# Optimization experiments

Hardware: AMD Instinct MI355X
Metric: run time of the kernel (lower is better)

The kernel has to match this reference:

```python
import jax, jax.numpy as jnp
import numpy as np

IMG_W, IMG_H = 960.0, 512.0   # image_size (w, h)
HM_W, HM_H = 240, 128         # heatmap_size (w, h)


def _bilinear(fmap, gx, gy):
    # fmap: [C,H,W]; gx, gy: [N] normalized coords; bilinear, align_corners=False, zero padding
    C, H, W = fmap.shape
    ix = (gx + 1.0) * W * 0.5 - 0.5
    iy = (gy + 1.0) * H * 0.5 - 0.5
    x0f = jnp.floor(ix); y0f = jnp.floor(iy)
    wx1 = ix - x0f; wy1 = iy - y0f

    def tap(xf, yf, wgt):
        valid = (xf >= 0) & (xf <= W - 1) & (yf >= 0) & (yf <= H - 1)
        xc = jnp.clip(xf.astype(jnp.int32), 0, W - 1)
        yc = jnp.clip(yf.astype(jnp.int32), 0, H - 1)
        return fmap[:, yc, xc] * (wgt * valid.astype(fmap.dtype))

    return (tap(x0f, y0f, (1 - wx1) * (1 - wy1)) + tap(x0f + 1, y0f, wx1 * (1 - wy1))
            + tap(x0f, y0f + 1, (1 - wx1) * wy1) + tap(x0f + 1, y0f + 1, wx1 * wy1))


def _forward(feature_maps, grid_center, space_center, space_size, sub_space_size,
             cube, centers, trans, cam_R, cam_T, cam_f, cam_c):
    n_cam, B, C, H, W = feature_maps.shape
    vox = jnp.float32(cube)
    fine_n = (space_size / sub_space_size * (vox - 1.0)).astype(jnp.int32) + 1   # [3]
    fine_nf = fine_n.astype(jnp.float32)
    scale = (fine_nf - 1.0) / space_size
    bias = (-sub_space_size / 2.0 / space_size * (fine_nf - 1.0)
            - scale * (space_center - space_size / 2.0))
    centers_tl = jnp.round(grid_center[:, :3] * scale + bias).astype(jnp.int32)  # [B,3]
    offset = (centers_tl.astype(jnp.float32) / (fine_nf - 1.0) * space_size
              - space_size / 2.0 + sub_space_size / 2.0)                          # [B,3]
    mask_xy = jnp.maximum(((1.0 - grid_center[:, 5:7]) / 2.0 * (vox - 1.0)).astype(jnp.int32), 0)
    mask = jnp.concatenate([mask_xy, jnp.zeros((B, 1), jnp.int32)], axis=1)       # [B,3]
    start = jnp.maximum(centers_tl + mask, 0)
    end = jnp.minimum(centers_tl + cube - mask, fine_n)
    end = jnp.maximum(end, start + 1)

    # fixed-size sub-cube of fine-grid indices; out-of-window cells are masked to 0
    v = jnp.arange(cube)
    mesh = jnp.stack(jnp.meshgrid(v, v, v, indexing="ij"), axis=-1).reshape(-1, 3)  # [N,3]
    fidx = centers_tl[:, None, :] + mesh[None]                                       # [B,N,3]
    valid = jnp.all((fidx >= start[:, None, :]) & (fidx < end[:, None, :]), axis=-1)  # [B,N]
    valid = valid & (grid_center[:, 3:4] >= 0)
    world = (space_center - space_size / 2.0
             + fidx.astype(jnp.float32) / (fine_nf - 1.0) * space_size)              # [B,N,3]

    # pinhole world->pixel per (batch, camera)
    rel = world[:, None, :, :] - cam_T[:, :, None, :]                                # [B,K,N,3]
    Xc = jnp.einsum("bkij,bknj->bkni", cam_R, rel)
    xy = cam_f[:, :, None, :] * Xc[..., :2] / Xc[..., 2:3] + cam_c[:, :, None, :]    # [B,K,N,2]
    maxwh = jnp.max(centers * 2.0, axis=-1)[:, :, None, None]
    xy = jnp.clip(xy, -1.0, maxwh)
    xy = jnp.einsum("bkij,bknj->bkni", trans[..., :2], xy) + trans[:, :, None, :, 2]  # affine crop
    xy = xy * jnp.array([HM_W / IMG_W, HM_H / IMG_H], jnp.float32)
    g = jnp.clip(xy / jnp.array([HM_W - 1.0, HM_H - 1.0], jnp.float32) * 2.0 - 1.0, -1.1, 1.1)

    fm = jnp.transpose(feature_maps, (1, 0, 2, 3, 4))                                # [B,K,C,H,W]
    samp = jax.vmap(jax.vmap(_bilinear))(fm, g[..., 0], g[..., 1])                   # [B,K,C,N]
    samp = samp * valid[:, None, None, :].astype(samp.dtype)
    cubes = jnp.sum(samp, axis=1) / (n_cam + 1e-6)            # mean agg (bounding==1)
    cubes = jnp.clip(cubes, 0.0, 1.0).reshape(B, C, cube, cube, cube)
    return cubes, offset


def setup_inputs() -> dict:
    key = jax.random.key(0)
    ks = jax.random.split(key, 10)
    n_cam, B, C, H, W = 5, 4, 15, 128, 240
    feature_maps = jax.random.uniform(ks[0], (n_cam, B, C, H, W), jnp.float32)
    xy = jax.random.uniform(ks[1], (B, 2), minval=-3000.0, maxval=3000.0)
    z = jax.random.uniform(ks[2], (B, 1), minval=800.0, maxval=1200.0)
    flag = jnp.ones((B, 2), jnp.float32)  # cols 3 (validity >= 0) and 4
    m = jax.random.uniform(ks[3], (B, 2), minval=0.6, maxval=1.0)  # cols 5:7 mask fracs
    grid_center = jnp.concatenate([xy, z, flag, m], axis=1)        # [B,7]
    space_center = jnp.array([0.0, 0.0, 1000.0], jnp.float32)
    space_size = jnp.array([8000.0, 8000.0, 2000.0], jnp.float32)
    sub_space_size = jnp.array([2000.0, 2000.0, 2000.0], jnp.float32)
    centers = jnp.array([IMG_W / 2, IMG_H / 2], jnp.float32) + \
        jax.random.uniform(ks[4], (B, n_cam, 2), minval=-5.0, maxval=5.0)
    base = jnp.array([[1.0, 0.0, 0.0], [0.0, 1.0, 0.0]], jnp.float32)
    trans = base + 0.01 * jax.random.normal(ks[5], (B, n_cam, 2, 3), jnp.float32)
    cam_R = jnp.eye(3, dtype=jnp.float32) + 0.05 * jax.random.normal(ks[6], (B, n_cam, 3, 3), jnp.float32)
    t_xy = jax.random.uniform(ks[7], (B, n_cam, 2), minval=-500.0, maxval=500.0)
    cam_T = jnp.concatenate([t_xy, jnp.full((B, n_cam, 1), -6000.0, jnp.float32)], axis=-1)
    cam_f = jax.random.uniform(ks[8], (B, n_cam, 2), minval=500.0, maxval=700.0)
    cam_c = jnp.array([IMG_W / 2, IMG_H / 2], jnp.float32) + \
        jax.random.uniform(ks[9], (B, n_cam, 2), minval=-10.0, maxval=10.0)
    return {"feature_maps": feature_maps, "grid_center": grid_center,
            "space_center": space_center, "space_size": space_size,
            "sub_space_size": sub_space_size, "sub_cube_size": 64,
            "centers": centers, "trans": trans, "cam_R": cam_R,
            "cam_T": cam_T, "cam_f": cam_f, "cam_c": cam_c}


def reference(feature_maps, grid_center, space_center, space_size, sub_space_size,
              sub_cube_size, centers, trans, cam_R, cam_T, cam_f, cam_c):
    return _forward(feature_maps, grid_center, space_center, space_size, sub_space_size,
                    int(sub_cube_size), centers, trans, cam_R, cam_T, cam_f, cam_c)
```

## Files before the change

### kernel.cpp

```cpp
#include <hip/hip_runtime.h>
#include <hip/hip_fp16.h>

#define NCAM 5
#define NC 15
#define NCP 16
#define FH 128
#define FW 240
#define HW (FH*FW)
#define CUBE 64
#define NVOX (CUBE*CUBE*CUBE)
#define THREADS 256
#define BLOCKS_PER_B (NVOX/THREADS)
#define CSTR 24

__global__ __launch_bounds__(THREADS) void transpose_fm(
    const float* __restrict__ fm, __half* __restrict__ fmH)
{
    const int p  = blockIdx.x * THREADS + threadIdx.x;
    const int cb = blockIdx.y;
    const float* src = fm + (size_t)cb * NC * HW + p;
    __half v[NCP];
    #pragma unroll
    for (int c = 0; c < NC; ++c) v[c] = __float2half(src[(size_t)c * HW]);
    v[15] = __float2half(0.0f);
    uint4* dst = (uint4*)(fmH + ((size_t)cb * HW + p) * NCP);
    dst[0] = *(const uint4*)(v);
    dst[1] = *(const uint4*)(v + 8);
}

__global__ void setup_kernel(
    const float* __restrict__ gc, const float* __restrict__ space_c,
    const float* __restrict__ space_s, const float* __restrict__ sub_s,
    const float* __restrict__ centers, const float* __restrict__ trans,
    const float* __restrict__ cam_R, const float* __restrict__ cam_T,
    const float* __restrict__ cam_f, const float* __restrict__ cam_c,
    float* __restrict__ camS, int* __restrict__ bwin,
    float* __restrict__ out, int B)
{
    const int t = threadIdx.x;
    if (t < B) {
        const int b = t;
        #pragma unroll
        for (int d = 0; d < 3; ++d) {
            float ssz = space_s[d], sc = space_c[d], sub = sub_s[d];
            int   fn  = (int)(ssz / sub * (CUBE - 1.0f)) + 1;
            float fnf = (float)fn;
            float scale = (fnf - 1.0f) / ssz;
            float bias  = -sub / 2.0f / ssz * (fnf - 1.0f) - scale * (sc - ssz / 2.0f);
            int ctl = (int)rintf(gc[b*7 + d] * scale + bias);
            int mask = 0;
            if (d < 2) {
                mask = (int)((1.0f - gc[b*7 + 5 + d]) / 2.0f * (CUBE - 1.0f));
                if (mask < 0) mask = 0;
            }
            int st = max(ctl + mask, 0);
            int en = min(ctl + CUBE - mask, fn);
            en = max(en, st + 1);
            bwin[b*12 + d]     = ctl;
            bwin[b*12 + 3 + d] = st;
            bwin[b*12 + 6 + d] = en;
            out[(size_t)B * NC * NVOX + b*3 + d] =
                (float)ctl / (fnf - 1.0f) * ssz - ssz / 2.0f + sub / 2.0f;
        }
        bwin[b*12 + 9] = (gc[b*7 + 3] >= 0.0f) ? 1 : 0;
    }
    if (t < B * NCAM) {
        const int b = t / NCAM, cam = t % NCAM, bk = b*NCAM + cam;
        float sA[3], bA[3];
        #pragma unroll
        for (int d = 0; d < 3; ++d) {
            float ssz = space_s[d], sub = sub_s[d];
            int   fn  = (int)(ssz / sub * (CUBE - 1.0f)) + 1;
            float fnf = (float)fn;
            sA[d] = ssz / (fnf - 1.0f);
            bA[d] = space_c[d] - ssz * 0.5f;
        }
        const float* R = cam_R + bk*9;
        const float* T = cam_T + bk*3;
        float* P = camS + (size_t)bk * CSTR;
        #pragma unroll
        for (int i = 0; i < 3; ++i) {
            #pragma unroll
            for (int d = 0; d < 3; ++d) P[i*3 + d] = R[i*3 + d] * sA[d];
            P[9 + i] = R[i*3+0]*(bA[0]-T[0]) + R[i*3+1]*(bA[1]-T[1]) + R[i*3+2]*(bA[2]-T[2]);
        }
        P[12] = cam_f[bk*2+0];  P[13] = cam_f[bk*2+1];
        P[14] = cam_c[bk*2+0];  P[15] = cam_c[bk*2+1];
        P[16] = fmaxf(centers[bk*2+0]*2.0f, centers[bk*2+1]*2.0f);
        const float* tr = trans + bk*6;
        const float KX = 60.0f/239.0f, KY = 32.0f/127.0f;
        P[17] = tr[0]*KX;  P[18] = tr[1]*KX;  P[19] = tr[2]*KX - 120.0f;
        P[20] = tr[3]*KY;  P[21] = tr[4]*KY;  P[22] = tr[5]*KY - 64.0f;
        P[23] = 0.0f;
    }
}

#define FMA_MIX2(lo, hi, wt, wrd)                                             \
    asm("v_fma_mix_f32 %0, %1, %2, %0 op_sel_hi:[0,1,0]"                      \
        : "+v"(lo) : "v"(wt), "v"(wrd));                                      \
    asm("v_fma_mix_f32 %0, %1, %2, %0 op_sel:[0,1,0] op_sel_hi:[0,1,0]"       \
        : "+v"(hi) : "v"(wt), "v"(wrd));

#define TAPFMA(wt, A, Bv)                                                     \
    FMA_MIX2(acc[0],  acc[1],  wt, A.x)                                       \
    FMA_MIX2(acc[2],  acc[3],  wt, A.y)                                       \
    FMA_MIX2(acc[4],  acc[5],  wt, A.z)                                       \
    FMA_MIX2(acc[6],  acc[7],  wt, A.w)                                       \
    FMA_MIX2(acc[8],  acc[9],  wt, Bv.x)                                      \
    FMA_MIX2(acc[10], acc[11], wt, Bv.y)                                      \
    FMA_MIX2(acc[12], acc[13], wt, Bv.z)                                      \
    FMA_MIX2(acc[14], acc[15], wt, Bv.w)

struct CamProj { unsigned o[4]; float w[4]; };

__device__ __forceinline__ CamProj projcam(const float* __restrict__ P,
                                           float fxf, float fyf, float fzf)
{
    float X0 = fmaf(P[0], fxf, fmaf(P[1], fyf, fmaf(P[2], fzf, P[9])));
    float X1 = fmaf(P[3], fxf, fmaf(P[4], fyf, fmaf(P[5], fzf, P[10])));
    float X2 = fmaf(P[6], fxf, fmaf(P[7], fyf, fmaf(P[8], fzf, P[11])));
    float rz = __builtin_amdgcn_rcpf(X2);
    float mw = P[16];
    float px = fmaf(P[12]*X0, rz, P[14]);
    float py = fmaf(P[13]*X1, rz, P[15]);
    px = fminf(fmaxf(px, -1.0f), mw);
    py = fminf(fmaxf(py, -1.0f), mw);
    float ixf = fminf(fmaxf(fmaf(P[17], px, fmaf(P[18], py, P[19])), -132.0f), 132.0f) + 119.5f;
    float iyf = fminf(fmaxf(fmaf(P[20], px, fmaf(P[21], py, P[22])), -70.4f), 70.4f) + 63.5f;
    float x0f = floorf(ixf), y0f = floorf(iyf);
    float wx1 = ixf - x0f,  wy1 = iyf - y0f;
    float wx0 = 1.0f - wx1, wy0 = 1.0f - wy1;
    int x0 = (int)x0f, y0 = (int)y0f, x1 = x0 + 1, y1 = y0 + 1;
    bool vx0 = (unsigned)x0 <= (FW-1), vx1 = (unsigned)x1 <= (FW-1);
    bool vy0 = (unsigned)y0 <= (FH-1), vy1 = (unsigned)y1 <= (FH-1);
    CamProj r;
    r.w[0] = (vx0 && vy0) ? wx0*wy0 : 0.0f;
    r.w[1] = (vx1 && vy0) ? wx1*wy0 : 0.0f;
    r.w[2] = (vx0 && vy1) ? wx0*wy1 : 0.0f;
    r.w[3] = (vx1 && vy1) ? wx1*wy1 : 0.0f;
    int xc0 = min(max(x0,0),FW-1), xc1 = min(max(x1,0),FW-1);
    int yc0 = min(max(y0,0),FH-1), yc1 = min(max(y1,0),FH-1);
    r.o[0] = (unsigned)(yc0*FW + xc0);  r.o[1] = (unsigned)(yc0*FW + xc1);
    r.o[2] = (unsigned)(yc1*FW + xc0);  r.o[3] = (unsigned)(yc1*FW + xc1);
    return r;
}

#define LOADC(CP, K, D)                                                       \
    { const __half* bp = fmH + (size_t)((K)*B + b) * HW * NCP;                \
      const uint4* q;                                                         \
      q = (const uint4*)(bp + (size_t)CP.o[0]*NCP); D[0]=q[0]; D[1]=q[1];     \
      q = (const uint4*)(bp + (size_t)CP.o[1]*NCP); D[2]=q[0]; D[3]=q[1];     \
      q = (const uint4*)(bp + (size_t)CP.o[2]*NCP); D[4]=q[0]; D[5]=q[1];     \
      q = (const uint4*)(bp + (size_t)CP.o[3]*NCP); D[6]=q[0]; D[7]=q[1]; }

#define FMAC(CP, D)                                                           \
    TAPFMA(CP.w[0], D[0], D[1])                                               \
    TAPFMA(CP.w[1], D[2], D[3])                                               \
    TAPFMA(CP.w[2], D[4], D[5])                                               \
    TAPFMA(CP.w[3], D[6], D[7])

__global__ __launch_bounds__(THREADS, 3) void proj_main(
    const __half* __restrict__ fmH,
    const float* __restrict__ camS,
    const int* __restrict__ bwin,
    float* __restrict__ out, int B)
{
    const int b = blockIdx.x / BLOCKS_PER_B;
    const int n = (blockIdx.x % BLOCKS_PER_B) * THREADS + threadIdx.x;
    const int vi = n >> 12, vj = (n >> 6) & 63, vk = n & 63;

    const int* W = bwin + b*12;
    const int fx = W[0] + vi, fy = W[1] + vj, fz = W[2] + vk;
    const bool valid = (fx >= W[3]) & (fx < W[6])
                     & (fy >= W[4]) & (fy < W[7])
                     & (fz >= W[5]) & (fz < W[8])
                     & (W[9] != 0);

    float acc[NCP];
    #pragma unroll
    for (int c = 0; c < NCP; ++c) acc[c] = 0.0f;

    if (valid) {
        const float fxf = (float)fx, fyf = (float)fy, fzf = (float)fz;
        const float* cs = camS + (size_t)(b*NCAM) * CSTR;
        uint4 d0[8], d1[8];

        CamProj cp0 = projcam(cs + 0*CSTR, fxf, fyf, fzf);
        LOADC(cp0, 0, d0)
        CamProj cp1 = projcam(cs + 1*CSTR, fxf, fyf, fzf);
        LOADC(cp1, 1, d1)
        CamProj cp2 = projcam(cs + 2*CSTR, fxf, fyf, fzf);
        FMAC(cp0, d0)
        LOADC(cp2, 2, d0)
        CamProj cp3 = projcam(cs + 3*CSTR, fxf, fyf, fzf);
        FMAC(cp1, d1)
        LOADC(cp3, 3, d1)
        CamProj cp4 = projcam(cs + 4*CSTR, fxf, fyf, fzf);
        FMAC(cp2, d0)
        LOADC(cp4, 4, d0)
        FMAC(cp3, d1)
        FMAC(cp4, d0)
    }

    const float RINV = 0.19999996000000800f;
    #pragma unroll
    for (int c = 0; c < NC; ++c) {
        float v = acc[c] * RINV;
        v = fminf(fmaxf(v, 0.0f), 1.0f);
        out[((size_t)(b*NC + c)) * NVOX + n] = v;
    }
}

__global__ __launch_bounds__(THREADS) void proj_fallback(
    const float* __restrict__ fm, const float* __restrict__ gc,
    const float* __restrict__ space_center, const float* __restrict__ space_size,
    const float* __restrict__ sub_size, const float* __restrict__ centers,
    const float* __restrict__ trans, const float* __restrict__ cam_R,
    const float* __restrict__ cam_T, const float* __restrict__ cam_f,
    const float* __restrict__ cam_c, float* __restrict__ out, int B)
{
    const int b = blockIdx.x / BLOCKS_PER_B;
    const int n = (blockIdx.x % BLOCKS_PER_B) * THREADS + threadIdx.x;
    float ctlf[3], fnf[3], sc[3], ssz[3];
    int   ctl[3], st[3], en[3];
    #pragma unroll
    for (int d = 0; d < 3; ++d) {
        ssz[d] = space_size[d];
        sc[d]  = space_center[d];
        float sub = sub_size[d];
        int fn = (int)(ssz[d] / sub * (CUBE - 1.0f)) + 1;
        fnf[d] = (float)fn;
        float scale = (fnf[d] - 1.0f) / ssz[d];
        float bias  = -sub / 2.0f / ssz[d] * (fnf[d] - 1.0f)
                      - scale * (sc[d] - ssz[d] / 2.0f);
        int c_tl = (int)rintf(gc[b*7 + d] * scale + bias);
        ctl[d]  = c_tl;  ctlf[d] = (float)c_tl;
        int mask = 0;
        if (d < 2) {
            mask = (int)((1.0f - gc[b*7 + 5 + d]) / 2.0f * (CUBE - 1.0f));
            if (mask < 0) mask = 0;
        }
        st[d] = max(c_tl + mask, 0);
        int e = min(c_tl + CUBE - mask, fn);
        en[d] = max(e, st[d] + 1);
    }
    if (n < 3) {
        int d = n;
        out[(size_t)B * NC * NVOX + b*3 + d] =
            ctlf[d] / (fnf[d] - 1.0f) * ssz[d] - ssz[d] / 2.0f + sub_size[d] / 2.0f;
    }
    const int vi = n >> 12, vj = (n >> 6) & 63, vk = n & 63;
    const int fx = ctl[0] + vi, fy = ctl[1] + vj, fz = ctl[2] + vk;
    const bool valid = (fx >= st[0]) & (fx < en[0]) & (fy >= st[1]) & (fy < en[1])
                     & (fz >= st[2]) & (fz < en[2]) & (gc[b*7 + 3] >= 0.0f);
    float acc[NC];
    #pragma unroll
    for (int c = 0; c < NC; ++c) acc[c] = 0.0f;
    if (valid) {
        const float wxw = sc[0] - ssz[0]*0.5f + (float)fx / (fnf[0]-1.0f) * ssz[0];
        const float wyw = sc[1] - ssz[1]*0.5f + (float)fy / (fnf[1]-1.0f) * ssz[1];
        const float wzw = sc[2] - ssz[2]*0.5f + (float)fz / (fnf[2]-1.0f) * ssz[2];
        for (int cam = 0; cam < NCAM; ++cam) {
            const int bk = b*NCAM + cam;
            const float* R = cam_R + bk*9;
            const float* T = cam_T + bk*3;
            float r0 = wxw - T[0], r1 = wyw - T[1], r2 = wzw - T[2];
            float X0 = R[0]*r0 + R[1]*r1 + R[2]*r2;
            float X1 = R[3]*r0 + R[4]*r1 + R[5]*r2;
            float X2 = R[6]*r0 + R[7]*r1 + R[8]*r2;
            float px = cam_f[bk*2+0]*X0/X2 + cam_c[bk*2+0];
            float py = cam_f[bk*2+1]*X1/X2 + cam_c[bk*2+1];
            float maxwh = fmaxf(centers[bk*2+0]*2.0f, centers[bk*2+1]*2.0f);
            px = fminf(fmaxf(px, -1.0f), maxwh);
            py = fminf(fmaxf(py, -1.0f), maxwh);
            const float* tr = trans + bk*6;
            float tx = (tr[0]*px + tr[1]*py + tr[2]) * 0.25f;
            float ty = (tr[3]*px + tr[4]*py + tr[5]) * 0.25f;
            float gx = fminf(fmaxf(tx/239.0f*2.0f - 1.0f, -1.1f), 1.1f);
            float gy = fminf(fmaxf(ty/127.0f*2.0f - 1.0f, -1.1f), 1.1f);
            float ixf = (gx + 1.0f)*(FW*0.5f) - 0.5f;
            float iyf = (gy + 1.0f)*(FH*0.5f) - 0.5f;
            float x0f = floorf(ixf), y0f = floorf(iyf);
            float wx1 = ixf - x0f,  wy1 = iyf - y0f;
            float wx0 = 1.0f - wx1, wy0 = 1.0f - wy1;
            int x0 = (int)x0f, y0 = (int)y0f, x1 = x0 + 1, y1 = y0 + 1;
            bool vx0 = (x0 >= 0) & (x0 <= FW-1), vx1 = (x1 >= 0) & (x1 <= FW-1);
            bool vy0 = (y0 >= 0) & (y0 <= FH-1), vy1 = (y1 >= 0) & (y1 <= FH-1);
            float w00 = wx0*wy0*(float)(vx0 & vy0);
            float w10 = wx1*wy0*(float)(vx1 & vy0);
            float w01 = wx0*wy1*(float)(vx0 & vy1);
            float w11 = wx1*wy1*(float)(vx1 & vy1);
            int xc0 = min(max(x0,0),FW-1), xc1 = min(max(x1,0),FW-1);
            int yc0 = min(max(y0,0),FH-1), yc1 = min(max(y1,0),FH-1);
            int o00 = yc0*FW + xc0, o10 = yc0*FW + xc1;
            int o01 = yc1*FW + xc0, o11 = yc1*FW + xc1;
            const float* base = fm + ((size_t)(cam*B + b)) * NC * HW;
            #pragma unroll
            for (int c = 0; c < NC; ++c) {
                const float* p = base + c*HW;
                acc[c] += w00*p[o00] + w10*p[o10] + w01*p[o01] + w11*p[o11];
            }
        }
    }
    const float invd = (float)(5.0 + 1e-6);
    #pragma unroll
    for (int c = 0; c < NC; ++c) {
        float v = acc[c] / invd;
        v = fminf(fmaxf(v, 0.0f), 1.0f);
        out[((size_t)(b*NC + c)) * NVOX + n] = v;
    }
}

extern "C" void kernel_launch(void* const* d_in, const int* in_sizes, int n_in,
                              void* d_out, int out_size, void* d_ws, size_t ws_size,
                              hipStream_t stream) {
    const float* fm        = (const float*)d_in[0];
    const float* gc        = (const float*)d_in[1];
    const float* space_c   = (const float*)d_in[2];
    const float* space_s   = (const float*)d_in[3];
    const float* sub_s     = (const float*)d_in[4];
    const float* centers   = (const float*)d_in[6];
    const float* trans     = (const float*)d_in[7];
    const float* cam_R     = (const float*)d_in[8];
    const float* cam_T     = (const float*)d_in[9];
    const float* cam_f     = (const float*)d_in[10];
    const float* cam_c     = (const float*)d_in[11];
    float* out = (float*)d_out;
    const int B = in_sizes[1] / 7;

    const size_t FMHB   = (size_t)NCAM * B * HW * NCP * sizeof(__half);
    const size_t CAMOFF = (FMHB + 255) & ~(size_t)255;
    const size_t BWOFF  = (CAMOFF + (size_t)B * NCAM * CSTR * 4 + 255) & ~(size_t)255;
    const size_t NEED   = BWOFF + (size_t)B * 48;

    if (ws_size >= NEED) {
        __half* fmH = (__half*)d_ws;
        float*  camS = (float*)((char*)d_ws + CAMOFF);
        int*    bwin = (int*)((char*)d_ws + BWOFF);
        hipLaunchKernelGGL(setup_kernel, dim3(1), dim3(256), 0, stream,
                           gc, space_c, space_s, sub_s, centers, trans,
                           cam_R, cam_T, cam_f, cam_c, camS, bwin, out, B);
        dim3 tg(HW / THREADS, NCAM * B);
        hipLaunchKernelGGL(transpose_fm, tg, dim3(THREADS), 0, stream, fm, fmH);
        dim3 grid(B * BLOCKS_PER_B), block(THREADS);
        hipLaunchKernelGGL(proj_main, grid, block, 0, stream,
                           fmH, camS, bwin, out, B);
    } else {
        dim3 grid(B * BLOCKS_PER_B), block(THREADS);
        hipLaunchKernelGGL(proj_fallback, grid, block, 0, stream,
                           fm, gc, space_c, space_s, sub_s,
                           centers, trans, cam_R, cam_T, cam_f, cam_c, out, B);
    }
}
```

Measured before the change: 46.34 us.

## Fuse setup into transpose, skip empty camera taps, enlarge projection blocks

Folds the setup kernel into block (0,0) of the transpose kernel, removing one launch. Replaces the manually double-buffered camera loop in the main projection kernel with a simple loop that skips a camera's gathers when no lane in the wavefront has a nonzero bilinear weight. It also raises the main kernel to 512 threads per block and drops the occupancy hint. The skip saves memory traffic for voxels that project outside an image, but it loses the software prefetch overlap between cameras.

```diff
diff --git a/kernel.cpp b/kernel.cpp
--- a/kernel.cpp
+++ b/kernel.cpp
@@ -9,26 +9,13 @@
 #define HW (FH*FW)
 #define CUBE 64
 #define NVOX (CUBE*CUBE*CUBE)
-#define THREADS 256
-#define BLOCKS_PER_B (NVOX/THREADS)
+#define MTHREADS 512
+#define MBLOCKS_PER_B (NVOX/MTHREADS)
+#define TTHREADS 256
 #define CSTR 24
 
-__global__ __launch_bounds__(THREADS) void transpose_fm(
-    const float* __restrict__ fm, __half* __restrict__ fmH)
-{
-    const int p  = blockIdx.x * THREADS + threadIdx.x;
-    const int cb = blockIdx.y;
-    const float* src = fm + (size_t)cb * NC * HW + p;
-    __half v[NCP];
-    #pragma unroll
-    for (int c = 0; c < NC; ++c) v[c] = __float2half(src[(size_t)c * HW]);
-    v[15] = __float2half(0.0f);
-    uint4* dst = (uint4*)(fmH + ((size_t)cb * HW + p) * NCP);
-    dst[0] = *(const uint4*)(v);
-    dst[1] = *(const uint4*)(v + 8);
-}
-
-__global__ void setup_kernel(
+__global__ __launch_bounds__(TTHREADS) void transpose_fm(
+    const float* __restrict__ fm, __half* __restrict__ fmH,
     const float* __restrict__ gc, const float* __restrict__ space_c,
     const float* __restrict__ space_s, const float* __restrict__ sub_s,
     const float* __restrict__ centers, const float* __restrict__ trans,
@@ -38,61 +25,73 @@
     float* __restrict__ out, int B)
 {
     const int t = threadIdx.x;
-    if (t < B) {
-        const int b = t;
-        #pragma unroll
-        for (int d = 0; d < 3; ++d) {
-            float ssz = space_s[d], sc = space_c[d], sub = sub_s[d];
-            int   fn  = (int)(ssz / sub * (CUBE - 1.0f)) + 1;
-            float fnf = (float)fn;
-            float scale = (fnf - 1.0f) / ssz;
-            float bias  = -sub / 2.0f / ssz * (fnf - 1.0f) - scale * (sc - ssz / 2.0f);
-            int ctl = (int)rintf(gc[b*7 + d] * scale + bias);
-            int mask = 0;
-            if (d < 2) {
-                mask = (int)((1.0f - gc[b*7 + 5 + d]) / 2.0f * (CUBE - 1.0f));
-                if (mask < 0) mask = 0;
-            }
-            int st = max(ctl + mask, 0);
-            int en = min(ctl + CUBE - mask, fn);
-            en = max(en, st + 1);
-            bwin[b*12 + d]     = ctl;
-            bwin[b*12 + 3 + d] = st;
-            bwin[b*12 + 6 + d] = en;
-            out[(size_t)B * NC * NVOX + b*3 + d] =
-                (float)ctl / (fnf - 1.0f) * ssz - ssz / 2.0f + sub / 2.0f;
-        }
-        bwin[b*12 + 9] = (gc[b*7 + 3] >= 0.0f) ? 1 : 0;
-    }
-    if (t < B * NCAM) {
-        const int b = t / NCAM, cam = t % NCAM, bk = b*NCAM + cam;
-        float sA[3], bA[3];
-        #pragma unroll
-        for (int d = 0; d < 3; ++d) {
-            float ssz = space_s[d], sub = sub_s[d];
-            int   fn  = (int)(ssz / sub * (CUBE - 1.0f)) + 1;
-            float fnf = (float)fn;
-            sA[d] = ssz / (fnf - 1.0f);
-            bA[d] = space_c[d] - ssz * 0.5f;
-        }
-        const float* R = cam_R + bk*9;
-        const float* T = cam_T + bk*3;
-        float* P = camS + (size_t)bk * CSTR;
-        #pragma unroll
-        for (int i = 0; i < 3; ++i) {
+    if (blockIdx.x == 0 && blockIdx.y == 0) {
+        if (t < B) {
+            const int b = t;
             #pragma unroll
-            for (int d = 0; d < 3; ++d) P[i*3 + d] = R[i*3 + d] * sA[d];
-            P[9 + i] = R[i*3+0]*(bA[0]-T[0]) + R[i*3+1]*(bA[1]-T[1]) + R[i*3+2]*(bA[2]-T[2]);
-        }
-        P[12] = cam_f[bk*2+0];  P[13] = cam_f[bk*2+1];
-        P[14] = cam_c[bk*2+0];  P[15] = cam_c[bk*2+1];
-        P[16] = fmaxf(centers[bk*2+0]*2.0f, centers[bk*2+1]*2.0f);
-        const float* tr = trans + bk*6;
-        const float KX = 60.0f/239.0f, KY = 32.0f/127.0f;
-        P[17] = tr[0]*KX;  P[18] = tr[1]*KX;  P[19] = tr[2]*KX - 120.0f;
-        P[20] = tr[3]*KY;  P[21] = tr[4]*KY;  P[22] = tr[5]*KY - 64.0f;
-        P[23] = 0.0f;
-    }
+            for (int d = 0; d < 3; ++d) {
+                float ssz = space_s[d], sc = space_c[d], sub = sub_s[d];
+                int   fn  = (int)(ssz / sub * (CUBE - 1.0f)) + 1;
+                float fnf = (float)fn;
+                float scale = (fnf - 1.0f) / ssz;
+                float bias  = -sub / 2.0f / ssz * (fnf - 1.0f) - scale * (sc - ssz / 2.0f);
+                int ctl = (int)rintf(gc[b*7 + d] * scale + bias);
+                int mask = 0;
+                if (d < 2) {
+                    mask = (int)((1.0f - gc[b*7 + 5 + d]) / 2.0f * (CUBE - 1.0f));
+                    if (mask < 0) mask = 0;
+                }
+                int st = max(ctl + mask, 0);
+                int en = min(ctl + CUBE - mask, fn);
+                en = max(en, st + 1);
+                bwin[b*12 + d]     = ctl;
+                bwin[b*12 + 3 + d] = st;
+                bwin[b*12 + 6 + d] = en;
+                out[(size_t)B * NC * NVOX + b*3 + d] =
+                    (float)ctl / (fnf - 1.0f) * ssz - ssz / 2.0f + sub / 2.0f;
+            }
+            bwin[t*12 + 9] = (gc[t*7 + 3] >= 0.0f) ? 1 : 0;
+        }
+        if (t < B * NCAM) {
+            const int b = t / NCAM, bk = t;
+            float sA[3], bA[3];
+            #pragma unroll
+            for (int d = 0; d < 3; ++d) {
+                float ssz = space_s[d], sub = sub_s[d];
+                int   fn  = (int)(ssz / sub * (CUBE - 1.0f)) + 1;
+                sA[d] = ssz / ((float)fn - 1.0f);
+                bA[d] = space_c[d] - ssz * 0.5f;
+            }
+            const float* R = cam_R + bk*9;
+            const float* T = cam_T + bk*3;
+            float* P = camS + (size_t)bk * CSTR;
+            #pragma unroll
+            for (int i = 0; i < 3; ++i) {
+                #pragma unroll
+                for (int d = 0; d < 3; ++d) P[i*3 + d] = R[i*3 + d] * sA[d];
+                P[9 + i] = R[i*3+0]*(bA[0]-T[0]) + R[i*3+1]*(bA[1]-T[1]) + R[i*3+2]*(bA[2]-T[2]);
+            }
+            P[12] = cam_f[bk*2+0];  P[13] = cam_f[bk*2+1];
+            P[14] = cam_c[bk*2+0];  P[15] = cam_c[bk*2+1];
+            P[16] = fmaxf(centers[bk*2+0]*2.0f, centers[bk*2+1]*2.0f);
+            const float* tr = trans + bk*6;
+            const float KX = 60.0f/239.0f, KY = 32.0f/127.0f;
+            P[17] = tr[0]*KX;  P[18] = tr[1]*KX;  P[19] = tr[2]*KX - 120.0f;
+            P[20] = tr[3]*KY;  P[21] = tr[4]*KY;  P[22] = tr[5]*KY - 64.0f;
+            P[23] = 0.0f;
+            (void)b;
+        }
+    }
+    const int p  = blockIdx.x * TTHREADS + t;
+    const int cb = blockIdx.y;
+    const float* src = fm + (size_t)cb * NC * HW + p;
+    __half v[NCP];
+    #pragma unroll
+    for (int c = 0; c < NC; ++c) v[c] = __float2half(src[(size_t)c * HW]);
+    v[15] = __float2half(0.0f);
+    uint4* dst = (uint4*)(fmH + ((size_t)cb * HW + p) * NCP);
+    dst[0] = *(const uint4*)(v);
+    dst[1] = *(const uint4*)(v + 8);
 }
 
 #define FMA_MIX2(lo, hi, wt, wrd)                                             \
@@ -145,28 +144,14 @@
     return r;
 }
 
-#define LOADC(CP, K, D)                                                       \
-    { const __half* bp = fmH + (size_t)((K)*B + b) * HW * NCP;                \
-      const uint4* q;                                                         \
-      q = (const uint4*)(bp + (size_t)CP.o[0]*NCP); D[0]=q[0]; D[1]=q[1];     \
-      q = (const uint4*)(bp + (size_t)CP.o[1]*NCP); D[2]=q[0]; D[3]=q[1];     \
-      q = (const uint4*)(bp + (size_t)CP.o[2]*NCP); D[4]=q[0]; D[5]=q[1];     \
-      q = (const uint4*)(bp + (size_t)CP.o[3]*NCP); D[6]=q[0]; D[7]=q[1]; }
-
-#define FMAC(CP, D)                                                           \
-    TAPFMA(CP.w[0], D[0], D[1])                                               \
-    TAPFMA(CP.w[1], D[2], D[3])                                               \
-    TAPFMA(CP.w[2], D[4], D[5])                                               \
-    TAPFMA(CP.w[3], D[6], D[7])
-
-__global__ __launch_bounds__(THREADS, 3) void proj_main(
+__global__ __launch_bounds__(MTHREADS) void proj_main(
     const __half* __restrict__ fmH,
     const float* __restrict__ camS,
     const int* __restrict__ bwin,
     float* __restrict__ out, int B)
 {
-    const int b = blockIdx.x / BLOCKS_PER_B;
-    const int n = (blockIdx.x % BLOCKS_PER_B) * THREADS + threadIdx.x;
+    const int b = blockIdx.x / MBLOCKS_PER_B;
+    const int n = (blockIdx.x % MBLOCKS_PER_B) * MTHREADS + threadIdx.x;
     const int vi = n >> 12, vj = (n >> 6) & 63, vk = n & 63;
 
     const int* W = bwin + b*12;
@@ -183,23 +168,26 @@
     if (valid) {
         const float fxf = (float)fx, fyf = (float)fy, fzf = (float)fz;
         const float* cs = camS + (size_t)(b*NCAM) * CSTR;
-        uint4 d0[8], d1[8];
-
-        CamProj cp0 = projcam(cs + 0*CSTR, fxf, fyf, fzf);
-        LOADC(cp0, 0, d0)
-        CamProj cp1 = projcam(cs + 1*CSTR, fxf, fyf, fzf);
-        LOADC(cp1, 1, d1)
-        CamProj cp2 = projcam(cs + 2*CSTR, fxf, fyf, fzf);
-        FMAC(cp0, d0)
-        LOADC(cp2, 2, d0)
-        CamProj cp3 = projcam(cs + 3*CSTR, fxf, fyf, fzf);
-        FMAC(cp1, d1)
-        LOADC(cp3, 3, d1)
-        CamProj cp4 = projcam(cs + 4*CSTR, fxf, fyf, fzf);
-        FMAC(cp2, d0)
-        LOADC(cp4, 4, d0)
-        FMAC(cp3, d1)
-        FMAC(cp4, d0)
+
+        #pragma unroll
+        for (int cam = 0; cam < NCAM; ++cam) {
+            CamProj cp = projcam(cs + cam*CSTR, fxf, fyf, fzf);
+            if (__any((cp.w[0] + cp.w[1] + cp.w[2] + cp.w[3]) != 0.0f)) {
+                const __half* bp = fmH + (size_t)(cam*B + b) * HW * NCP;
+                const uint4* q0 = (const uint4*)(bp + (size_t)cp.o[0]*NCP);
+                const uint4* q1 = (const uint4*)(bp + (size_t)cp.o[1]*NCP);
+                const uint4* q2 = (const uint4*)(bp + (size_t)cp.o[2]*NCP);
+                const uint4* q3 = (const uint4*)(bp + (size_t)cp.o[3]*NCP);
+                uint4 a0 = q0[0], b0 = q0[1];
+                uint4 a1 = q1[0], b1 = q1[1];
+                uint4 a2 = q2[0], b2 = q2[1];
+                uint4 a3 = q3[0], b3 = q3[1];
+                TAPFMA(cp.w[0], a0, b0)
+                TAPFMA(cp.w[1], a1, b1)
+                TAPFMA(cp.w[2], a2, b2)
+                TAPFMA(cp.w[3], a3, b3)
+            }
+        }
     }
 
     const float RINV = 0.19999996000000800f;
@@ -211,7 +199,7 @@
     }
 }
 
-__global__ __launch_bounds__(THREADS) void proj_fallback(
+__global__ __launch_bounds__(256) void proj_fallback(
     const float* __restrict__ fm, const float* __restrict__ gc,
     const float* __restrict__ space_center, const float* __restrict__ space_size,
     const float* __restrict__ sub_size, const float* __restrict__ centers,
@@ -219,8 +207,8 @@
     const float* __restrict__ cam_T, const float* __restrict__ cam_f,
     const float* __restrict__ cam_c, float* __restrict__ out, int B)
 {
-    const int b = blockIdx.x / BLOCKS_PER_B;
-    const int n = (blockIdx.x % BLOCKS_PER_B) * THREADS + threadIdx.x;
+    const int b = blockIdx.x / (NVOX/256);
+    const int n = (blockIdx.x % (NVOX/256)) * 256 + threadIdx.x;
     float ctlf[3], fnf[3], sc[3], ssz[3];
     int   ctl[3], st[3], en[3];
     #pragma unroll
@@ -334,19 +322,18 @@
     const size_t NEED   = BWOFF + (size_t)B * 48;
 
     if (ws_size >= NEED) {
-        __half* fmH = (__half*)d_ws;
+        __half* fmH  = (__half*)d_ws;
         float*  camS = (float*)((char*)d_ws + CAMOFF);
         int*    bwin = (int*)((char*)d_ws + BWOFF);
-        hipLaunchKernelGGL(setup_kernel, dim3(1), dim3(256), 0, stream,
-                           gc, space_c, space_s, sub_s, centers, trans,
+        dim3 tg(HW / TTHREADS, NCAM * B);
+        hipLaunchKernelGGL(transpose_fm, tg, dim3(TTHREADS), 0, stream,
+                           fm, fmH, gc, space_c, space_s, sub_s, centers, trans,
                            cam_R, cam_T, cam_f, cam_c, camS, bwin, out, B);
-        dim3 tg(HW / THREADS, NCAM * B);
-        hipLaunchKernelGGL(transpose_fm, tg, dim3(THREADS), 0, stream, fm, fmH);
-        dim3 grid(B * BLOCKS_PER_B), block(THREADS);
+        dim3 grid(B * MBLOCKS_PER_B), block(MTHREADS);
         hipLaunchKernelGGL(proj_main, grid, block, 0, stream,
                            fmH, camS, bwin, out, B);
     } else {
-        dim3 grid(B * BLOCKS_PER_B), block(THREADS);
+        dim3 grid(B * (NVOX/256)), block(256);
         hipLaunchKernelGGL(proj_fallback, grid, block, 0, stream,
                            fm, gc, space_c, space_s, sub_s,
                            centers, trans, cam_R, cam_T, cam_f, cam_c, out, B);
```

Result: no change. 45.48 us (-1.9%).
